# Kernel tuning notes

Measured on AMD Instinct MI355X. Metric: run time of the kernel, lower is better.

## Reference

```python
import jax, jax.numpy as jnp
import numpy as np

D_MODEL = 1024
NUM_HEADS = 16
NUM_KV_HEADS = 4
D_K = D_MODEL // NUM_HEADS              # 64
G = NUM_HEADS // NUM_KV_HEADS           # queries per kv head = 4
B, S = 2, 2048


def setup_inputs() -> dict:
    key = jax.random.key(0)
    ks = jax.random.split(key, 11)
    s = 0.02
    return {
        "query": jax.random.normal(ks[0], (B, S, D_MODEL), jnp.float32),
        "key_in": jax.random.normal(ks[1], (B, S, D_MODEL), jnp.float32),
        "value_in": jax.random.normal(ks[2], (B, S, D_MODEL), jnp.float32),
        "Wq": jax.random.normal(ks[3], (D_MODEL, D_MODEL), jnp.float32) * s,
        "bq": jnp.zeros((D_MODEL,), jnp.float32),
        "Wk": jax.random.normal(ks[4], (D_MODEL, NUM_KV_HEADS * D_K), jnp.float32) * s,
        "bk": jnp.zeros((NUM_KV_HEADS * D_K,), jnp.float32),
        "Wv": jax.random.normal(ks[5], (D_MODEL, NUM_KV_HEADS * D_K), jnp.float32) * s,
        "bv": jnp.zeros((NUM_KV_HEADS * D_K,), jnp.float32),
        "Wo": jax.random.normal(ks[6], (D_MODEL, D_MODEL), jnp.float32) * s,
        "bo": jnp.zeros((D_MODEL,), jnp.float32),
    }


def reference(query, key_in, value_in, Wq, bq, Wk, bk, Wv, bv, Wo, bo):
    scale = jnp.sqrt(jnp.asarray(D_K, query.dtype))
    # Projections
    Q = (query @ Wq + bq).reshape(B, S, NUM_HEADS, D_K).transpose(0, 2, 1, 3)        # [B,H,S,dk]
    K = (key_in @ Wk + bk).reshape(B, S, NUM_KV_HEADS, D_K).transpose(0, 2, 1, 3)    # [B,KVH,S,dk]
    V = (value_in @ Wv + bv).reshape(B, S, NUM_KV_HEADS, D_K).transpose(0, 2, 1, 3)  # [B,KVH,S,dk]
    # repeat_interleave over head dim -> group Q heads by KV head instead
    Qg = Q.reshape(B, NUM_KV_HEADS, G, S, D_K)                                       # [B,KVH,G,S,dk]
    scores = jnp.einsum('bkgqd,bksd->bkgqs', Qg, K) / scale                          # [B,KVH,G,S,S]
    attn = jax.nn.softmax(scores, axis=-1)
    ctx = jnp.einsum('bkgqs,bksd->bkgqd', attn, V)                                   # [B,KVH,G,S,dk]
    ctx = ctx.reshape(B, NUM_HEADS, S, D_K).transpose(0, 2, 1, 3).reshape(B, S, D_MODEL)
    output = ctx @ Wo + bo
    # new_cache: K[:, ::G] on the repeated tensor == original K/V per kv head
    return output, K, V
```

## Files before the change

### kernel.cpp

```cpp
#include <hip/hip_runtime.h>

typedef unsigned short u16;
typedef unsigned int u32;
typedef __attribute__((ext_vector_type(8))) short short8;
typedef __attribute__((ext_vector_type(4))) float f32x4;

#define MFMA16(a, b, c) __builtin_amdgcn_mfma_f32_16x16x32_bf16(a, b, c, 0, 0, 0)

#define SEQ 2048
#define DM 1024

__device__ __forceinline__ u16 f2bf(float f) {
  u32 u = __float_as_uint(f);
  u += 0x7fffu + ((u >> 16) & 1u);
  return (u16)(u >> 16);
}
__device__ __forceinline__ u32 pack2(float a, float b) {
  u32 r;
  asm("v_cvt_pk_bf16_f32 %0, %1, %2" : "=v"(r) : "v"(a), "v"(b));
  return r;
}
__device__ __forceinline__ u32 pack2t(float a, float b) {
  return __builtin_amdgcn_perm(__float_as_uint(b), __float_as_uint(a), 0x07060302u);
}
__device__ __forceinline__ uint4 cvt8(const float* f) {
  float4 a = *(const float4*)f;
  float4 b = *(const float4*)(f + 4);
  uint4 r;
  r.x = pack2(a.x, a.y);
  r.y = pack2(a.z, a.w);
  r.z = pack2(b.x, b.y);
  r.w = pack2(b.z, b.w);
  return r;
}
__device__ __forceinline__ void gload16(const u16* g, u16* l) {
  __builtin_amdgcn_global_load_lds((const __attribute__((address_space(1))) u32*)g,
                                   (__attribute__((address_space(3))) u32*)l, 16, 0, 0);
}

__global__ void k_tr(const float* __restrict__ Wq, const float* __restrict__ Wk,
                     const float* __restrict__ Wv, const float* __restrict__ Wo,
                     u16* __restrict__ WqT, u16* __restrict__ WkT, u16* __restrict__ WvT,
                     u16* __restrict__ WoT) {
  const int z = blockIdx.z;
  const float* W = z == 0 ? Wq : (z == 1 ? Wk : (z == 2 ? Wv : Wo));
  u16* Wt = z == 0 ? WqT : (z == 1 ? WkT : (z == 2 ? WvT : WoT));
  const int N = (z == 1 || z == 2) ? 256 : 1024;
  const int n0 = blockIdx.x * 32;
  if (n0 >= N) return;
  const int k0 = blockIdx.y * 32;
  __shared__ float tile[32][33];
  int x = threadIdx.x & 31, y = threadIdx.x >> 5;
#pragma unroll
  for (int i = 0; i < 4; i++)
    tile[y + i * 8][x] = W[(size_t)(k0 + y + i * 8) * N + n0 + x];
  __syncthreads();
#pragma unroll
  for (int i = 0; i < 4; i++)
    Wt[(size_t)(n0 + y + i * 8) * 1024 + k0 + x] = f2bf(tile[x][y + i * 8]);
}

template <bool A32, bool B32>
__device__ __forceinline__ void gemm64(const void* __restrict__ A, const void* __restrict__ Bt,
                                       int m0, int n0, u16* lA, u16* lB, f32x4 acc[2][4]) {
  const int tid = threadIdx.x;
  const int lane = tid & 63, wave = tid >> 6;
  const int l15 = lane & 15, quad = lane >> 4;
  const int wm = wave >> 1, wn = wave & 1;
  const int sr = tid >> 3, scol = (tid & 7) * 8;
  f32x4 zero = {0.f, 0.f, 0.f, 0.f};
#pragma unroll
  for (int i = 0; i < 2; i++)
#pragma unroll
    for (int j = 0; j < 4; j++) acc[i][j] = zero;

  for (int k0 = 0; k0 < 1024; k0 += 64) {
    if constexpr (A32) {
      const float* Af = (const float*)A;
#pragma unroll
      for (int it = 0; it < 2; it++) {
        int r = sr + it * 32;
        uint4 v = cvt8(Af + (size_t)(m0 + r) * 1024 + k0 + scol);
        *(uint4*)&lA[r * 64 + (((tid & 7) ^ (r & 7)) << 3)] = v;
      }
    } else {
      const u16* Ab = (const u16*)A;
#pragma unroll
      for (int it = 0; it < 2; it++) {
        int w8 = wave * 2 + it;
        int r = w8 * 8 + (lane >> 3);
        int g = (lane & 7) ^ (lane >> 3);
        gload16(Ab + (size_t)(m0 + r) * 1024 + k0 + g * 8, &lA[w8 * 512]);
      }
    }
    if constexpr (B32) {
      const float* Bf = (const float*)Bt;
#pragma unroll
      for (int it = 0; it < 4; it++) {
        int r = sr + it * 32;
        uint4 v = cvt8(Bf + (size_t)(n0 + r) * 1024 + k0 + scol);
        *(uint4*)&lB[r * 64 + (((tid & 7) ^ (r & 7)) << 3)] = v;
      }
    } else {
      const u16* Bb = (const u16*)Bt;
#pragma unroll
      for (int it = 0; it < 4; it++) {
        int w8 = wave * 4 + it;
        int r = w8 * 8 + (lane >> 3);
        int g = (lane & 7) ^ (lane >> 3);
        gload16(Bb + (size_t)(n0 + r) * 1024 + k0 + g * 8, &lB[w8 * 512]);
      }
    }
    __syncthreads();
    short8 af[2][2], bfr[4][2];
#pragma unroll
    for (int i = 0; i < 2; i++)
#pragma unroll
      for (int kb = 0; kb < 2; kb++) {
        int r = wm * 32 + i * 16 + l15;
        af[i][kb] = *(const short8*)&lA[r * 64 + (((kb * 4 + quad) ^ (r & 7)) << 3)];
      }
#pragma unroll
    for (int j = 0; j < 4; j++)
#pragma unroll
      for (int kb = 0; kb < 2; kb++) {
        int r = wn * 64 + j * 16 + l15;
        bfr[j][kb] = *(const short8*)&lB[r * 64 + (((kb * 4 + quad) ^ (r & 7)) << 3)];
      }
#pragma unroll
    for (int i = 0; i < 2; i++)
#pragma unroll
      for (int j = 0; j < 4; j++) {
        acc[i][j] = MFMA16(af[i][0], bfr[j][0], acc[i][j]);
        acc[i][j] = MFMA16(af[i][1], bfr[j][1], acc[i][j]);
      }
    __syncthreads();
  }
}

__global__ __launch_bounds__(256) void k_proj(
    const float* __restrict__ query, const float* __restrict__ key_in,
    const float* __restrict__ value_in, const u16* __restrict__ WqT,
    const u16* __restrict__ WkT, const u16* __restrict__ WvT, const float* __restrict__ bq,
    const float* __restrict__ bk, const float* __restrict__ bv, u16* __restrict__ qbf,
    float* __restrict__ outK, u16* __restrict__ kbf, float* __restrict__ outV,
    u16* __restrict__ vtb, float qscale) {
  __shared__ u16 lA[64 * 64];
  __shared__ u16 lB[128 * 64];
  const int idx = blockIdx.x;
  const int lane = threadIdx.x & 63, wave = threadIdx.x >> 6;
  const int l15 = lane & 15, quad = lane >> 4;
  const int wm = wave >> 1, wn = wave & 1;
  f32x4 acc[2][4];

  if (idx < 640) {
    const u16* Wt;
    const float* act;
    const float* bias;
    int m0, n0, mode;
    if (idx < 512) {
      Wt = WqT; act = query; bias = bq; m0 = (idx >> 5) * 64; n0 = (idx & 31) * 128; mode = 0;
    } else {
      int i2 = idx - 512;
      Wt = WkT; act = key_in; bias = bk; m0 = (i2 >> 5) * 64; n0 = (i2 & 31) * 128; mode = 1;
    }
    gemm64<false, true>(Wt, act, m0, n0, lA, lB, acc);
#pragma unroll
    for (int i = 0; i < 2; i++) {
      int c0 = m0 + wm * 32 + i * 16 + quad * 4;
      float4 bb = *(const float4*)(bias + c0);
#pragma unroll
      for (int j = 0; j < 4; j++) {
        int token = n0 + wn * 64 + j * 16 + l15;
        int b = token >> 11, s = token & 2047;
        float v0 = acc[i][j][0] + bb.x, v1 = acc[i][j][1] + bb.y;
        float v2 = acc[i][j][2] + bb.z, v3 = acc[i][j][3] + bb.w;
        int d = c0 & 63;
        if (mode == 0) {
          int h = c0 >> 6;
          uint2 o;
          o.x = pack2(v0 * qscale, v1 * qscale);
          o.y = pack2(v2 * qscale, v3 * qscale);
          *(uint2*)(qbf + (((size_t)(b * 16 + h) * SEQ + s) << 6) + d) = o;
        } else {
          int kvh = c0 >> 6;
          size_t ix = (((size_t)(b * 4 + kvh) * SEQ + s) << 6) + d;
          float4 vv = {v0, v1, v2, v3};
          *(float4*)(outK + ix) = vv;
          uint2 o;
          o.x = pack2(v0, v1);
          o.y = pack2(v2, v3);
          *(uint2*)(kbf + ix) = o;
        }
      }
    }
  } else {
    int i2 = idx - 640;
    int m0 = (i2 >> 1) * 64, n0 = (i2 & 1) * 128;
    gemm64<true, false>(value_in, WvT, m0, n0, lA, lB, acc);
#pragma unroll
    for (int i = 0; i < 2; i++) {
      int r0 = m0 + wm * 32 + i * 16 + quad * 4;
      int b = r0 >> 11, s0 = r0 & 2047;
#pragma unroll
      for (int j = 0; j < 4; j++) {
        int col = n0 + wn * 64 + j * 16 + l15;
        int kvh = col >> 6, d = col & 63;
        float bv_ = bv[col];
        float v0 = acc[i][j][0] + bv_, v1 = acc[i][j][1] + bv_;
        float v2 = acc[i][j][2] + bv_, v3 = acc[i][j][3] + bv_;
        size_t base = (((size_t)(b * 4 + kvh) * SEQ + s0) << 6) + d;
        outV[base] = v0;
        outV[base + 64] = v1;
        outV[base + 128] = v2;
        outV[base + 192] = v3;
        uint2 o;
        o.x = pack2(v0, v1);
        o.y = pack2(v2, v3);
        *(uint2*)(vtb + ((size_t)(b * 4 + kvh) * 64 + d) * SEQ + s0) = o;
      }
    }
  }
}

__global__ __launch_bounds__(256) void k_out(const u16* __restrict__ ctxb,
                                             const u16* __restrict__ WoT,
                                             const float* __restrict__ bo,
                                             float* __restrict__ out) {
  __shared__ u16 lA[64 * 64];
  __shared__ u16 lB[128 * 64];
  const int idx = blockIdx.x;
  const int m0 = (idx >> 5) * 64, n0 = (idx & 31) * 128;
  const int lane = threadIdx.x & 63, wave = threadIdx.x >> 6;
  const int l15 = lane & 15, quad = lane >> 4;
  const int wm = wave >> 1, wn = wave & 1;
  f32x4 acc[2][4];
  gemm64<false, false>(WoT, ctxb, m0, n0, lA, lB, acc);
#pragma unroll
  for (int i = 0; i < 2; i++) {
    int c0 = m0 + wm * 32 + i * 16 + quad * 4;
    float4 bb = *(const float4*)(bo + c0);
#pragma unroll
    for (int j = 0; j < 4; j++) {
      int token = n0 + wn * 64 + j * 16 + l15;
      float4 vv = {acc[i][j][0] + bb.x, acc[i][j][1] + bb.y, acc[i][j][2] + bb.z,
                   acc[i][j][3] + bb.w};
      *(float4*)(out + (size_t)token * DM + c0) = vv;
    }
  }
}

__global__ __launch_bounds__(256, 4) void k_flash(const u16* __restrict__ Qh,
                                                  const u16* __restrict__ Kb,
                                                  const u16* __restrict__ Vt,
                                                  u16* __restrict__ ctx) {
  __shared__ u16 lK[128 * 64];
  __shared__ u16 lV[64 * 128];
  __shared__ u16 lP[4 * 16 * 64];
  const int tid = threadIdx.x;
  const int lane = tid & 63, wave = tid >> 6;
  const int l15 = lane & 15, quad = lane >> 4;
  const int bh = blockIdx.y;
  const int b = bh >> 4, h = bh & 15, kvh = h >> 2;
  const u16* Q = Qh + (size_t)bh * SEQ * 64;
  const u16* Kp = Kb + (size_t)(b * 4 + kvh) * SEQ * 64;
  const u16* Vp = Vt + (size_t)(b * 4 + kvh) * 64 * SEQ;
  const int q0 = blockIdx.x * 64 + wave * 16;

  short8 qf[2];
#pragma unroll
  for (int kb = 0; kb < 2; kb++)
    qf[kb] = *(const short8*)(Q + (size_t)(q0 + l15) * 64 + kb * 32 + quad * 8);

  short8 ones8;
  {
    short ov = (l15 == 0) ? (short)0x3F80 : (short)0;
    ones8 = (short8){ov, ov, ov, ov, ov, ov, ov, ov};
  }

  f32x4 zero = {0.f, 0.f, 0.f, 0.f};
  f32x4 acc[4];
  f32x4 lacc = zero;
#pragma unroll
  for (int n = 0; n < 4; n++) acc[n] = zero;

  u16* lPw = lP + wave * (16 * 64);
  const int t8 = tid * 8;

  for (int kc = 0; kc < SEQ; kc += 128) {
    __syncthreads();
#pragma unroll
    for (int i = 0; i < 4; i++) {
      int e = i * 2048 + t8;
      int row = e >> 6, ch = tid & 7;
      uint4 v = *(const uint4*)(Kp + (size_t)kc * 64 + e);
      *(uint4*)&lK[row * 64 + ((ch ^ (row & 7)) << 3)] = v;
    }
#pragma unroll
    for (int i = 0; i < 4; i++) {
      int e = i * 2048 + t8;
      int row = e >> 7, ch = tid & 15;
      uint4 v = *(const uint4*)(Vp + (size_t)row * SEQ + kc + ch * 8);
      *(uint4*)&lV[row * 128 + ((ch ^ (row & 15)) << 3)] = v;
    }
    __syncthreads();

#pragma unroll
    for (int sub = 0; sub < 2; sub++) {
      const int ks = sub * 64;
      f32x4 sc[4];
#pragma unroll
      for (int mt = 0; mt < 4; mt++) {
        int row = ks + mt * 16 + l15;
        short8 kf0 = *(const short8*)&lK[row * 64 + ((quad ^ (row & 7)) << 3)];
        short8 kf1 = *(const short8*)&lK[row * 64 + (((4 + quad) ^ (row & 7)) << 3)];
        f32x4 t = MFMA16(kf0, qf[0], zero);
        sc[mt] = MFMA16(kf1, qf[1], t);
      }
#pragma unroll
      for (int mt = 0; mt < 4; mt++) {
        float e0 = __builtin_amdgcn_exp2f(sc[mt][0]);
        float e1 = __builtin_amdgcn_exp2f(sc[mt][1]);
        float e2 = __builtin_amdgcn_exp2f(sc[mt][2]);
        float e3 = __builtin_amdgcn_exp2f(sc[mt][3]);
        int chp = mt * 2 + (quad >> 1);
        uint2 p;
        p.x = pack2t(e0, e1);
        p.y = pack2t(e2, e3);
        *(uint2*)&lPw[l15 * 64 + ((chp ^ (l15 & 7)) << 3) + (quad & 1) * 4] = p;
      }
      __asm__ volatile("s_waitcnt lgkmcnt(0)" ::: "memory");
#pragma unroll
      for (int kbp = 0; kbp < 2; kbp++) {
        int chq = kbp * 4 + quad;
        short8 pf = *(const short8*)&lPw[l15 * 64 + ((chq ^ (l15 & 7)) << 3)];
        lacc = MFMA16(ones8, pf, lacc);
#pragma unroll
        for (int n = 0; n < 4; n++) {
          int row = n * 16 + l15;
          int chv = sub * 8 + kbp * 4 + quad;
          short8 vf = *(const short8*)&lV[row * 128 + ((chv ^ (row & 15)) << 3)];
          acc[n] = MFMA16(vf, pf, acc[n]);
        }
      }
    }
  }

  float lq = __shfl(lacc[0], l15);
  float inv = __builtin_amdgcn_rcpf(lq);
  u16* base = ctx + ((size_t)(b * SEQ + q0 + l15)) * DM + h * 64;
#pragma unroll
  for (int n = 0; n < 4; n++) {
    uint2 o;
    o.x = pack2t(acc[n][0] * inv, acc[n][1] * inv);
    o.y = pack2t(acc[n][2] * inv, acc[n][3] * inv);
    *(uint2*)(base + n * 16 + quad * 4) = o;
  }
}

extern "C" void kernel_launch(void* const* d_in, const int* in_sizes, int n_in,
                              void* d_out, int out_size, void* d_ws, size_t ws_size,
                              hipStream_t stream) {
  const float* query = (const float*)d_in[0];
  const float* key_in = (const float*)d_in[1];
  const float* value_in = (const float*)d_in[2];
  const float* Wq = (const float*)d_in[3];
  const float* bq = (const float*)d_in[4];
  const float* Wk = (const float*)d_in[5];
  const float* bk = (const float*)d_in[6];
  const float* Wv = (const float*)d_in[7];
  const float* bv = (const float*)d_in[8];
  const float* Wo = (const float*)d_in[9];
  const float* bo = (const float*)d_in[10];

  float* out = (float*)d_out;
  float* outK = out + 4194304;
  float* outV = out + 5242880;

  char* ws = (char*)d_ws;
  u16* WqT = (u16*)(ws);
  u16* WkT = (u16*)(ws + 2097152);
  u16* WvT = (u16*)(ws + 2621440);
  u16* WoT = (u16*)(ws + 3145728);
  u16* qbf = (u16*)(ws + 5242880);
  u16* kbf = (u16*)(ws + 13631488);
  u16* vtb = (u16*)(ws + 15728640);
  u16* ctxb = (u16*)(ws + 17825792);

  const float qscale = 0.125f * 1.44269504088896340736f;

  k_tr<<<dim3(32, 32, 4), 256, 0, stream>>>(Wq, Wk, Wv, Wo, WqT, WkT, WvT, WoT);
  k_proj<<<dim3(768), 256, 0, stream>>>(query, key_in, value_in, WqT, WkT, WvT, bq, bk, bv,
                                        qbf, outK, kbf, outV, vtb, qscale);
  k_flash<<<dim3(32, 32), 256, 0, stream>>>(qbf, kbf, vtb, ctxb);
  k_out<<<dim3(512), 256, 0, stream>>>(ctxb, WoT, bo, out);
}
```

Before: 210.6 us.

## Enlarge GEMM tiles to 128x128 with double-buffered LDS prefetch and block swizzle

Replaces the 64x128 single-buffered GEMM helper used by the projection and output kernels with a 128x128 tile version. It double-buffers LDS and issues the next k-slice's global loads (register-staged for fp32 inputs, direct-to-LDS for bf16) before the current MFMAs. Block indices are remapped so neighbouring blocks share operand tiles, and grids are halved to match the larger tiles. This aims to cut global traffic per FLOP and hide load latency, at the cost of more LDS and registers (launch bounds of 2) and fewer blocks in flight.

```diff
diff --git a/kernel.cpp b/kernel.cpp
--- a/kernel.cpp
+++ b/kernel.cpp
@@ -23,20 +23,12 @@
 __device__ __forceinline__ u32 pack2t(float a, float b) {
   return __builtin_amdgcn_perm(__float_as_uint(b), __float_as_uint(a), 0x07060302u);
 }
-__device__ __forceinline__ uint4 cvt8(const float* f) {
-  float4 a = *(const float4*)f;
-  float4 b = *(const float4*)(f + 4);
-  uint4 r;
-  r.x = pack2(a.x, a.y);
-  r.y = pack2(a.z, a.w);
-  r.z = pack2(b.x, b.y);
-  r.w = pack2(b.z, b.w);
-  return r;
-}
 __device__ __forceinline__ void gload16(const u16* g, u16* l) {
   __builtin_amdgcn_global_load_lds((const __attribute__((address_space(1))) u32*)g,
                                    (__attribute__((address_space(3))) u32*)l, 16, 0, 0);
 }
+
+struct f32x8v { float4 a, b; };
 
 __global__ void k_tr(const float* __restrict__ Wq, const float* __restrict__ Wk,
                      const float* __restrict__ Wv, const float* __restrict__ Wo,
@@ -61,117 +53,170 @@
 }
 
 template <bool A32, bool B32>
-__device__ __forceinline__ void gemm64(const void* __restrict__ A, const void* __restrict__ Bt,
-                                       int m0, int n0, u16* lA, u16* lB, f32x4 acc[2][4]) {
+__device__ __forceinline__ void gemm128(const void* __restrict__ A, const void* __restrict__ B,
+                                        u16* lA, u16* lB, f32x4 acc[4][4]) {
   const int tid = threadIdx.x;
   const int lane = tid & 63, wave = tid >> 6;
   const int l15 = lane & 15, quad = lane >> 4;
   const int wm = wave >> 1, wn = wave & 1;
-  const int sr = tid >> 3, scol = (tid & 7) * 8;
+  const int sr = tid >> 3, sch = tid & 7;
+  const int srow = lane >> 3;
+  const int g = (lane & 7) ^ srow;
   f32x4 zero = {0.f, 0.f, 0.f, 0.f};
 #pragma unroll
-  for (int i = 0; i < 2; i++)
+  for (int i = 0; i < 4; i++)
 #pragma unroll
     for (int j = 0; j < 4; j++) acc[i][j] = zero;
 
-  for (int k0 = 0; k0 < 1024; k0 += 64) {
+  f32x8v ra[4], rb[4];
+
+  auto issueA = [&](int k0, u16* dst) {
     if constexpr (A32) {
-      const float* Af = (const float*)A;
-#pragma unroll
-      for (int it = 0; it < 2; it++) {
+      const float* Af = (const float*)A + k0;
+#pragma unroll
+      for (int it = 0; it < 4; it++) {
+        const float* p = Af + (size_t)(sr + it * 32) * 1024 + sch * 8;
+        ra[it].a = *(const float4*)p;
+        ra[it].b = *(const float4*)(p + 4);
+      }
+    } else {
+      const u16* Ab = (const u16*)A + k0;
+#pragma unroll
+      for (int it = 0; it < 4; it++) {
+        int slab = wave * 4 + it;
+        gload16(Ab + (size_t)(slab * 8 + srow) * 1024 + g * 8, dst + slab * 512);
+      }
+    }
+  };
+  auto issueB = [&](int k0, u16* dst) {
+    if constexpr (B32) {
+      const float* Bf = (const float*)B + k0;
+#pragma unroll
+      for (int it = 0; it < 4; it++) {
+        const float* p = Bf + (size_t)(sr + it * 32) * 1024 + sch * 8;
+        rb[it].a = *(const float4*)p;
+        rb[it].b = *(const float4*)(p + 4);
+      }
+    } else {
+      const u16* Bb = (const u16*)B + k0;
+#pragma unroll
+      for (int it = 0; it < 4; it++) {
+        int slab = wave * 4 + it;
+        gload16(Bb + (size_t)(slab * 8 + srow) * 1024 + g * 8, dst + slab * 512);
+      }
+    }
+  };
+  auto writeA = [&](u16* dst) {
+    if constexpr (A32) {
+#pragma unroll
+      for (int it = 0; it < 4; it++) {
         int r = sr + it * 32;
-        uint4 v = cvt8(Af + (size_t)(m0 + r) * 1024 + k0 + scol);
-        *(uint4*)&lA[r * 64 + (((tid & 7) ^ (r & 7)) << 3)] = v;
-      }
-    } else {
-      const u16* Ab = (const u16*)A;
-#pragma unroll
-      for (int it = 0; it < 2; it++) {
-        int w8 = wave * 2 + it;
-        int r = w8 * 8 + (lane >> 3);
-        int g = (lane & 7) ^ (lane >> 3);
-        gload16(Ab + (size_t)(m0 + r) * 1024 + k0 + g * 8, &lA[w8 * 512]);
-      }
-    }
+        uint4 v;
+        v.x = pack2(ra[it].a.x, ra[it].a.y);
+        v.y = pack2(ra[it].a.z, ra[it].a.w);
+        v.z = pack2(ra[it].b.x, ra[it].b.y);
+        v.w = pack2(ra[it].b.z, ra[it].b.w);
+        *(uint4*)&dst[r * 64 + ((sch ^ (r & 7)) << 3)] = v;
+      }
+    }
+  };
+  auto writeB = [&](u16* dst) {
     if constexpr (B32) {
-      const float* Bf = (const float*)Bt;
 #pragma unroll
       for (int it = 0; it < 4; it++) {
         int r = sr + it * 32;
-        uint4 v = cvt8(Bf + (size_t)(n0 + r) * 1024 + k0 + scol);
-        *(uint4*)&lB[r * 64 + (((tid & 7) ^ (r & 7)) << 3)] = v;
-      }
-    } else {
-      const u16* Bb = (const u16*)Bt;
-#pragma unroll
-      for (int it = 0; it < 4; it++) {
-        int w8 = wave * 4 + it;
-        int r = w8 * 8 + (lane >> 3);
-        int g = (lane & 7) ^ (lane >> 3);
-        gload16(Bb + (size_t)(n0 + r) * 1024 + k0 + g * 8, &lB[w8 * 512]);
-      }
+        uint4 v;
+        v.x = pack2(rb[it].a.x, rb[it].a.y);
+        v.y = pack2(rb[it].a.z, rb[it].a.w);
+        v.z = pack2(rb[it].b.x, rb[it].b.y);
+        v.w = pack2(rb[it].b.z, rb[it].b.w);
+        *(uint4*)&dst[r * 64 + ((sch ^ (r & 7)) << 3)] = v;
+      }
+    }
+  };
+
+  issueA(0, lA);
+  issueB(0, lB);
+  writeA(lA);
+  writeB(lB);
+  __syncthreads();
+
+  int cur = 0;
+  for (int t = 0; t < 16; t++) {
+    u16* cA = lA + cur * 8192;
+    u16* cB = lB + cur * 8192;
+    u16* nA = lA + (cur ^ 1) * 8192;
+    u16* nB = lB + (cur ^ 1) * 8192;
+    if (t < 15) {
+      issueA((t + 1) * 64, nA);
+      issueB((t + 1) * 64, nB);
+    }
+    short8 af[4][2], bf[4][2];
+#pragma unroll
+    for (int i = 0; i < 4; i++) {
+      int r = wm * 64 + i * 16 + l15;
+#pragma unroll
+      for (int kb = 0; kb < 2; kb++)
+        af[i][kb] = *(const short8*)&cA[r * 64 + (((kb * 4 + quad) ^ (r & 7)) << 3)];
+    }
+#pragma unroll
+    for (int j = 0; j < 4; j++) {
+      int r = wn * 64 + j * 16 + l15;
+#pragma unroll
+      for (int kb = 0; kb < 2; kb++)
+        bf[j][kb] = *(const short8*)&cB[r * 64 + (((kb * 4 + quad) ^ (r & 7)) << 3)];
+    }
+#pragma unroll
+    for (int i = 0; i < 4; i++)
+#pragma unroll
+      for (int j = 0; j < 4; j++) {
+        acc[i][j] = MFMA16(af[i][0], bf[j][0], acc[i][j]);
+        acc[i][j] = MFMA16(af[i][1], bf[j][1], acc[i][j]);
+      }
+    if (t < 15) {
+      writeA(nA);
+      writeB(nB);
     }
     __syncthreads();
-    short8 af[2][2], bfr[4][2];
-#pragma unroll
-    for (int i = 0; i < 2; i++)
-#pragma unroll
-      for (int kb = 0; kb < 2; kb++) {
-        int r = wm * 32 + i * 16 + l15;
-        af[i][kb] = *(const short8*)&lA[r * 64 + (((kb * 4 + quad) ^ (r & 7)) << 3)];
-      }
-#pragma unroll
-    for (int j = 0; j < 4; j++)
-#pragma unroll
-      for (int kb = 0; kb < 2; kb++) {
-        int r = wn * 64 + j * 16 + l15;
-        bfr[j][kb] = *(const short8*)&lB[r * 64 + (((kb * 4 + quad) ^ (r & 7)) << 3)];
-      }
-#pragma unroll
-    for (int i = 0; i < 2; i++)
-#pragma unroll
-      for (int j = 0; j < 4; j++) {
-        acc[i][j] = MFMA16(af[i][0], bfr[j][0], acc[i][j]);
-        acc[i][j] = MFMA16(af[i][1], bfr[j][1], acc[i][j]);
-      }
-    __syncthreads();
-  }
-}
-
-__global__ __launch_bounds__(256) void k_proj(
+    cur ^= 1;
+  }
+}
+
+__global__ __launch_bounds__(256, 2) void k_proj(
     const float* __restrict__ query, const float* __restrict__ key_in,
     const float* __restrict__ value_in, const u16* __restrict__ WqT,
     const u16* __restrict__ WkT, const u16* __restrict__ WvT, const float* __restrict__ bq,
     const float* __restrict__ bk, const float* __restrict__ bv, u16* __restrict__ qbf,
     float* __restrict__ outK, u16* __restrict__ kbf, float* __restrict__ outV,
     u16* __restrict__ vtb, float qscale) {
-  __shared__ u16 lA[64 * 64];
-  __shared__ u16 lB[128 * 64];
-  const int idx = blockIdx.x;
+  __shared__ u16 lA[2 * 128 * 64];
+  __shared__ u16 lB[2 * 128 * 64];
+  const int bid = blockIdx.x;
+  const int idx = (bid & 7) * 48 + (bid >> 3);
   const int lane = threadIdx.x & 63, wave = threadIdx.x >> 6;
   const int l15 = lane & 15, quad = lane >> 4;
   const int wm = wave >> 1, wn = wave & 1;
-  f32x4 acc[2][4];
-
-  if (idx < 640) {
+  f32x4 acc[4][4];
+
+  if (idx < 320) {
     const u16* Wt;
     const float* act;
     const float* bias;
-    int m0, n0, mode;
-    if (idx < 512) {
-      Wt = WqT; act = query; bias = bq; m0 = (idx >> 5) * 64; n0 = (idx & 31) * 128; mode = 0;
+    int cm, tn, mode;
+    if (idx < 256) {
+      Wt = WqT; act = query; bias = bq; tn = (idx >> 3) * 128; cm = (idx & 7) * 128; mode = 0;
     } else {
-      int i2 = idx - 512;
-      Wt = WkT; act = key_in; bias = bk; m0 = (i2 >> 5) * 64; n0 = (i2 & 31) * 128; mode = 1;
-    }
-    gemm64<false, true>(Wt, act, m0, n0, lA, lB, acc);
-#pragma unroll
-    for (int i = 0; i < 2; i++) {
-      int c0 = m0 + wm * 32 + i * 16 + quad * 4;
+      int i2 = idx - 256;
+      Wt = WkT; act = key_in; bias = bk; tn = (i2 >> 1) * 128; cm = (i2 & 1) * 128; mode = 1;
+    }
+    gemm128<false, true>(Wt + (size_t)cm * 1024, act + (size_t)tn * 1024, lA, lB, acc);
+#pragma unroll
+    for (int i = 0; i < 4; i++) {
+      int c0 = cm + wm * 64 + i * 16 + quad * 4;
       float4 bb = *(const float4*)(bias + c0);
 #pragma unroll
       for (int j = 0; j < 4; j++) {
-        int token = n0 + wn * 64 + j * 16 + l15;
+        int token = tn + wn * 64 + j * 16 + l15;
         int b = token >> 11, s = token & 2047;
         float v0 = acc[i][j][0] + bb.x, v1 = acc[i][j][1] + bb.y;
         float v2 = acc[i][j][2] + bb.z, v3 = acc[i][j][3] + bb.w;
@@ -195,16 +240,17 @@
       }
     }
   } else {
-    int i2 = idx - 640;
-    int m0 = (i2 >> 1) * 64, n0 = (i2 & 1) * 128;
-    gemm64<true, false>(value_in, WvT, m0, n0, lA, lB, acc);
-#pragma unroll
-    for (int i = 0; i < 2; i++) {
-      int r0 = m0 + wm * 32 + i * 16 + quad * 4;
+    int i2 = idx - 320;
+    int tm = (i2 >> 1) * 128, cn = (i2 & 1) * 128;
+    gemm128<true, false>((const float*)value_in + (size_t)tm * 1024, WvT + (size_t)cn * 1024,
+                         lA, lB, acc);
+#pragma unroll
+    for (int i = 0; i < 4; i++) {
+      int r0 = tm + wm * 64 + i * 16 + quad * 4;
       int b = r0 >> 11, s0 = r0 & 2047;
 #pragma unroll
       for (int j = 0; j < 4; j++) {
-        int col = n0 + wn * 64 + j * 16 + l15;
+        int col = cn + wn * 64 + j * 16 + l15;
         int kvh = col >> 6, d = col & 63;
         float bv_ = bv[col];
         float v0 = acc[i][j][0] + bv_, v1 = acc[i][j][1] + bv_;
@@ -223,26 +269,27 @@
   }
 }
 
-__global__ __launch_bounds__(256) void k_out(const u16* __restrict__ ctxb,
-                                             const u16* __restrict__ WoT,
-                                             const float* __restrict__ bo,
-                                             float* __restrict__ out) {
-  __shared__ u16 lA[64 * 64];
-  __shared__ u16 lB[128 * 64];
-  const int idx = blockIdx.x;
-  const int m0 = (idx >> 5) * 64, n0 = (idx & 31) * 128;
+__global__ __launch_bounds__(256, 2) void k_out(const u16* __restrict__ ctxb,
+                                                const u16* __restrict__ WoT,
+                                                const float* __restrict__ bo,
+                                                float* __restrict__ out) {
+  __shared__ u16 lA[2 * 128 * 64];
+  __shared__ u16 lB[2 * 128 * 64];
+  const int bid = blockIdx.x;
+  const int idx = (bid & 7) * 32 + (bid >> 3);
+  const int tn = (idx >> 3) * 128, cm = (idx & 7) * 128;
   const int lane = threadIdx.x & 63, wave = threadIdx.x >> 6;
   const int l15 = lane & 15, quad = lane >> 4;
   const int wm = wave >> 1, wn = wave & 1;
-  f32x4 acc[2][4];
-  gemm64<false, false>(WoT, ctxb, m0, n0, lA, lB, acc);
-#pragma unroll
-  for (int i = 0; i < 2; i++) {
-    int c0 = m0 + wm * 32 + i * 16 + quad * 4;
+  f32x4 acc[4][4];
+  gemm128<false, false>(WoT + (size_t)cm * 1024, ctxb + (size_t)tn * 1024, lA, lB, acc);
+#pragma unroll
+  for (int i = 0; i < 4; i++) {
+    int c0 = cm + wm * 64 + i * 16 + quad * 4;
     float4 bb = *(const float4*)(bo + c0);
 #pragma unroll
     for (int j = 0; j < 4; j++) {
-      int token = n0 + wn * 64 + j * 16 + l15;
+      int token = tn + wn * 64 + j * 16 + l15;
       float4 vv = {acc[i][j][0] + bb.x, acc[i][j][1] + bb.y, acc[i][j][2] + bb.z,
                    acc[i][j][3] + bb.w};
       *(float4*)(out + (size_t)token * DM + c0) = vv;
@@ -390,8 +437,8 @@
   const float qscale = 0.125f * 1.44269504088896340736f;
 
   k_tr<<<dim3(32, 32, 4), 256, 0, stream>>>(Wq, Wk, Wv, Wo, WqT, WkT, WvT, WoT);
-  k_proj<<<dim3(768), 256, 0, stream>>>(query, key_in, value_in, WqT, WkT, WvT, bq, bk, bv,
+  k_proj<<<dim3(384), 256, 0, stream>>>(query, key_in, value_in, WqT, WkT, WvT, bq, bk, bv,
                                         qbf, outK, kbf, outV, vtb, qscale);
   k_flash<<<dim3(32, 32), 256, 0, stream>>>(qbf, kbf, vtb, ctxb);
-  k_out<<<dim3(512), 256, 0, stream>>>(ctxb, WoT, bo, out);
-}
+  k_out<<<dim3(256), 256, 0, stream>>>(ctxb, WoT, bo, out);
+}
```

Measured after the change: 222.4 us. +5.6%, slower.

## Process two query tiles per wave in flash kernel with direct-to-LDS K/V loads

Applied to the files above, without the earlier changes.

Each wave now handles 32 query rows (two 16-row groups) instead of 16, so every K and V fragment read from LDS feeds two MFMAs and each block covers 128 queries, halving the grid. K/V tile staging switches to a gload16 helper that copies global memory straight into LDS, with the swizzle applied on the global address. This cuts LDS reads and global K/V traffic per query. The cost is doubled accumulator registers, occupancy lowered to 2 blocks per CU, and only 512 blocks to fill the GPU.

```diff
diff --git a/kernel.cpp b/kernel.cpp
--- a/kernel.cpp
+++ b/kernel.cpp
@@ -250,13 +250,13 @@
   }
 }
 
-__global__ __launch_bounds__(256, 4) void k_flash(const u16* __restrict__ Qh,
+__global__ __launch_bounds__(256, 2) void k_flash(const u16* __restrict__ Qh,
                                                   const u16* __restrict__ Kb,
                                                   const u16* __restrict__ Vt,
                                                   u16* __restrict__ ctx) {
   __shared__ u16 lK[128 * 64];
   __shared__ u16 lV[64 * 128];
-  __shared__ u16 lP[4 * 16 * 64];
+  __shared__ u16 lP[4 * 32 * 64];
   const int tid = threadIdx.x;
   const int lane = tid & 63, wave = tid >> 6;
   const int l15 = lane & 15, quad = lane >> 4;
@@ -265,12 +265,14 @@
   const u16* Q = Qh + (size_t)bh * SEQ * 64;
   const u16* Kp = Kb + (size_t)(b * 4 + kvh) * SEQ * 64;
   const u16* Vp = Vt + (size_t)(b * 4 + kvh) * 64 * SEQ;
-  const int q0 = blockIdx.x * 64 + wave * 16;
-
-  short8 qf[2];
-#pragma unroll
-  for (int kb = 0; kb < 2; kb++)
-    qf[kb] = *(const short8*)(Q + (size_t)(q0 + l15) * 64 + kb * 32 + quad * 8);
+  const int q0 = blockIdx.x * 128 + wave * 32;
+
+  short8 qf[2][2];
+#pragma unroll
+  for (int g = 0; g < 2; g++)
+#pragma unroll
+    for (int kb = 0; kb < 2; kb++)
+      qf[g][kb] = *(const short8*)(Q + (size_t)(q0 + g * 16 + l15) * 64 + kb * 32 + quad * 8);
 
   short8 ones8;
   {
@@ -279,82 +281,93 @@
   }
 
   f32x4 zero = {0.f, 0.f, 0.f, 0.f};
-  f32x4 acc[4];
-  f32x4 lacc = zero;
-#pragma unroll
-  for (int n = 0; n < 4; n++) acc[n] = zero;
-
-  u16* lPw = lP + wave * (16 * 64);
-  const int t8 = tid * 8;
+  f32x4 acc[2][4];
+  f32x4 lacc[2] = {zero, zero};
+#pragma unroll
+  for (int g = 0; g < 2; g++)
+#pragma unroll
+    for (int n = 0; n < 4; n++) acc[g][n] = zero;
+
+  u16* lPw = lP + wave * (32 * 64);
+  const int gr3 = lane >> 3, gc7 = lane & 7;
+  const int gr4 = lane >> 4, gc15 = lane & 15;
 
   for (int kc = 0; kc < SEQ; kc += 128) {
     __syncthreads();
 #pragma unroll
     for (int i = 0; i < 4; i++) {
-      int e = i * 2048 + t8;
-      int row = e >> 6, ch = tid & 7;
-      uint4 v = *(const uint4*)(Kp + (size_t)kc * 64 + e);
-      *(uint4*)&lK[row * 64 + ((ch ^ (row & 7)) << 3)] = v;
+      int slab = wave * 4 + i;
+      gload16(Kp + (size_t)(kc + slab * 8 + gr3) * 64 + ((gc7 ^ gr3) << 3), lK + slab * 512);
     }
 #pragma unroll
     for (int i = 0; i < 4; i++) {
-      int e = i * 2048 + t8;
-      int row = e >> 7, ch = tid & 15;
-      uint4 v = *(const uint4*)(Vp + (size_t)row * SEQ + kc + ch * 8);
-      *(uint4*)&lV[row * 128 + ((ch ^ (row & 15)) << 3)] = v;
+      int slab = wave * 4 + i;
+      int row = slab * 4 + gr4;
+      gload16(Vp + (size_t)row * SEQ + kc + ((gc15 ^ (row & 15)) << 3), lV + slab * 512);
     }
     __syncthreads();
 
 #pragma unroll
     for (int sub = 0; sub < 2; sub++) {
       const int ks = sub * 64;
-      f32x4 sc[4];
+      f32x4 sc[2][4];
 #pragma unroll
       for (int mt = 0; mt < 4; mt++) {
         int row = ks + mt * 16 + l15;
         short8 kf0 = *(const short8*)&lK[row * 64 + ((quad ^ (row & 7)) << 3)];
         short8 kf1 = *(const short8*)&lK[row * 64 + (((4 + quad) ^ (row & 7)) << 3)];
-        f32x4 t = MFMA16(kf0, qf[0], zero);
-        sc[mt] = MFMA16(kf1, qf[1], t);
-      }
-#pragma unroll
-      for (int mt = 0; mt < 4; mt++) {
-        float e0 = __builtin_amdgcn_exp2f(sc[mt][0]);
-        float e1 = __builtin_amdgcn_exp2f(sc[mt][1]);
-        float e2 = __builtin_amdgcn_exp2f(sc[mt][2]);
-        float e3 = __builtin_amdgcn_exp2f(sc[mt][3]);
-        int chp = mt * 2 + (quad >> 1);
-        uint2 p;
-        p.x = pack2t(e0, e1);
-        p.y = pack2t(e2, e3);
-        *(uint2*)&lPw[l15 * 64 + ((chp ^ (l15 & 7)) << 3) + (quad & 1) * 4] = p;
-      }
+#pragma unroll
+        for (int g = 0; g < 2; g++) {
+          f32x4 t = MFMA16(kf0, qf[g][0], zero);
+          sc[g][mt] = MFMA16(kf1, qf[g][1], t);
+        }
+      }
+#pragma unroll
+      for (int g = 0; g < 2; g++)
+#pragma unroll
+        for (int mt = 0; mt < 4; mt++) {
+          float e0 = __builtin_amdgcn_exp2f(sc[g][mt][0]);
+          float e1 = __builtin_amdgcn_exp2f(sc[g][mt][1]);
+          float e2 = __builtin_amdgcn_exp2f(sc[g][mt][2]);
+          float e3 = __builtin_amdgcn_exp2f(sc[g][mt][3]);
+          int chp = mt * 2 + (quad >> 1);
+          uint2 p;
+          p.x = pack2t(e0, e1);
+          p.y = pack2t(e2, e3);
+          *(uint2*)&lPw[(g * 16 + l15) * 64 + ((chp ^ (l15 & 7)) << 3) + (quad & 1) * 4] = p;
+        }
       __asm__ volatile("s_waitcnt lgkmcnt(0)" ::: "memory");
 #pragma unroll
       for (int kbp = 0; kbp < 2; kbp++) {
         int chq = kbp * 4 + quad;
-        short8 pf = *(const short8*)&lPw[l15 * 64 + ((chq ^ (l15 & 7)) << 3)];
-        lacc = MFMA16(ones8, pf, lacc);
+        short8 pf0 = *(const short8*)&lPw[l15 * 64 + ((chq ^ (l15 & 7)) << 3)];
+        short8 pf1 = *(const short8*)&lPw[(16 + l15) * 64 + ((chq ^ (l15 & 7)) << 3)];
+        lacc[0] = MFMA16(ones8, pf0, lacc[0]);
+        lacc[1] = MFMA16(ones8, pf1, lacc[1]);
 #pragma unroll
         for (int n = 0; n < 4; n++) {
           int row = n * 16 + l15;
           int chv = sub * 8 + kbp * 4 + quad;
           short8 vf = *(const short8*)&lV[row * 128 + ((chv ^ (row & 15)) << 3)];
-          acc[n] = MFMA16(vf, pf, acc[n]);
+          acc[0][n] = MFMA16(vf, pf0, acc[0][n]);
+          acc[1][n] = MFMA16(vf, pf1, acc[1][n]);
         }
       }
     }
   }
 
-  float lq = __shfl(lacc[0], l15);
-  float inv = __builtin_amdgcn_rcpf(lq);
-  u16* base = ctx + ((size_t)(b * SEQ + q0 + l15)) * DM + h * 64;
-#pragma unroll
-  for (int n = 0; n < 4; n++) {
-    uint2 o;
-    o.x = pack2t(acc[n][0] * inv, acc[n][1] * inv);
-    o.y = pack2t(acc[n][2] * inv, acc[n][3] * inv);
-    *(uint2*)(base + n * 16 + quad * 4) = o;
+#pragma unroll
+  for (int g = 0; g < 2; g++) {
+    float lq = __shfl(lacc[g][0], l15);
+    float inv = __builtin_amdgcn_rcpf(lq);
+    u16* base = ctx + ((size_t)(b * SEQ + q0 + g * 16 + l15)) * DM + h * 64;
+#pragma unroll
+    for (int n = 0; n < 4; n++) {
+      uint2 o;
+      o.x = pack2t(acc[g][n][0] * inv, acc[g][n][1] * inv);
+      o.y = pack2t(acc[g][n][2] * inv, acc[g][n][3] * inv);
+      *(uint2*)(base + n * 16 + quad * 4) = o;
+    }
   }
 }
 
@@ -392,6 +405,6 @@
   k_tr<<<dim3(32, 32, 4), 256, 0, stream>>>(Wq, Wk, Wv, Wo, WqT, WkT, WvT, WoT);
   k_proj<<<dim3(768), 256, 0, stream>>>(query, key_in, value_in, WqT, WkT, WvT, bq, bk, bv,
                                         qbf, outK, kbf, outV, vtb, qscale);
-  k_flash<<<dim3(32, 32), 256, 0, stream>>>(qbf, kbf, vtb, ctxb);
+  k_flash<<<dim3(16, 32), 256, 0, stream>>>(qbf, kbf, vtb, ctxb);
   k_out<<<dim3(512), 256, 0, stream>>>(ctxb, WoT, bo, out);
 }
```

After: 205.5 us. -2.4%, faster.
